# Kernel optimization log

Measured on AMD Instinct MI355X. Metric: run time of the kernel, lower is better.

The kernel has to match this reference:

```python
import jax, jax.numpy as jnp
import numpy as np

N_NODES = 100000
N_EDGES = 3200000
IN_CH = 512
HID = 16
OUT_CH = 2


def setup_inputs() -> dict:
    key = jax.random.key(0)
    k1, k2, k3, k4 = jax.random.split(key, 4)
    x = jax.random.normal(k1, (N_NODES, IN_CH), dtype=jnp.float32)
    edge_index = jax.random.randint(k2, (2, N_EDGES), 0, N_NODES, dtype=jnp.int32)
    # GCNConv weight (glorot-style scale) and zero bias; Linear xavier weight, zero bias
    W1 = jax.random.normal(k3, (IN_CH, HID), dtype=jnp.float32) * np.float32(np.sqrt(2.0 / (IN_CH + HID)))
    b1 = jnp.zeros((HID,), dtype=jnp.float32)
    W2 = jax.random.normal(k4, (HID, OUT_CH), dtype=jnp.float32) * np.float32(np.sqrt(2.0 / (HID + OUT_CH)))
    b2 = jnp.zeros((OUT_CH,), dtype=jnp.float32)
    return {"x": x, "edge_index": edge_index, "W1": W1, "b1": b1, "W2": W2, "b2": b2}


def reference(x, edge_index, W1, b1, W2, b2):
    # GCNConv with default add_self_loops=True, normalize=True:
    #   out = D^{-1/2} (A + I) D^{-1/2} X W1 + b1, then Linear(16, out).
    n = x.shape[0]
    loops = jnp.arange(n, dtype=edge_index.dtype)
    row = jnp.concatenate([edge_index[0], loops])  # source nodes j
    col = jnp.concatenate([edge_index[1], loops])  # target nodes i
    deg = jax.ops.segment_sum(jnp.ones_like(col, dtype=x.dtype), col, num_segments=n)
    dinv = jnp.where(deg > 0, jax.lax.rsqrt(deg), jnp.zeros_like(deg))
    norm = dinv[row] * dinv[col]  # [E+N]
    xw = x @ W1  # [N, 16] project first (PyG GCNConv order)
    agg = jax.ops.segment_sum(xw[row] * norm[:, None], col, num_segments=n)  # scatter-add to targets
    h = agg + b1
    return h @ W2 + b2  # [N, out_channels]
```

## Files before the change

kernel.cpp:

```cpp
#include <hip/hip_runtime.h>


constexpr int N_NODES = 100000;
constexpr int N_EDGES = 3200000;
constexpr int IN_CH   = 512;
constexpr int HID     = 16;
constexpr int OUT_CH  = 2;

constexpr int NBUCK      = (N_NODES + 255) / 256;
constexpr int BIN_BLOCKS = 320;
constexpr int EPB        = N_EDGES / BIN_BLOCKS;
constexpr int XW_BLOCKS  = N_NODES / 32;

typedef __attribute__((ext_vector_type(4))) float floatx4;


__global__ __launch_bounds__(1024) void k_count_wc(const int* __restrict__ tgt,
                                                   int* __restrict__ hist,
                                                   const float* __restrict__ W1,
                                                   const float* __restrict__ b1,
                                                   const float* __restrict__ W2,
                                                   const float* __restrict__ b2,
                                                   float* __restrict__ Wc,
                                                   float* __restrict__ bconst) {
    if (blockIdx.x == BIN_BLOCKS) {
        for (int i = threadIdx.x; i < IN_CH * OUT_CH; i += 1024) {
            int c = i >> 1, o = i & 1;
            float s = 0.f;
#pragma unroll
            for (int h = 0; h < HID; ++h) s += W1[c * HID + h] * W2[h * OUT_CH + o];
            Wc[i] = s;
        }
        if (threadIdx.x < OUT_CH) {
            float bo = b2[threadIdx.x];
#pragma unroll
            for (int h = 0; h < HID; ++h) bo += b1[h] * W2[h * OUT_CH + threadIdx.x];
            bconst[threadIdx.x] = bo;
        }
        return;
    }
    __shared__ int h[NBUCK];
    for (int i = threadIdx.x; i < NBUCK; i += 1024) h[i] = 0;
    __syncthreads();
    int e0 = blockIdx.x * EPB;
    for (int e = e0 + threadIdx.x; e < e0 + EPB; e += 1024)
        atomicAdd(&h[tgt[e] >> 8], 1);
    __syncthreads();
    for (int i = threadIdx.x; i < NBUCK; i += 1024)
        hist[blockIdx.x * NBUCK + i] = h[i];
}

__global__ __launch_bounds__(64) void k_colscan(int* __restrict__ hist,
                                                int* __restrict__ coltot) {
    int b = blockIdx.x;
    int lane = threadIdx.x;
    int v[5];
    int s = 0;
#pragma unroll
    for (int j = 0; j < 5; ++j) {
        v[j] = hist[(lane * 5 + j) * NBUCK + b];
        s += v[j];
    }
    int inc = s;
#pragma unroll
    for (int off = 1; off < 64; off <<= 1) {
        int n = __shfl_up(inc, off);
        if (lane >= off) inc += n;
    }
    int excl = inc - s;
#pragma unroll
    for (int j = 0; j < 5; ++j) {
        hist[(lane * 5 + j) * NBUCK + b] = excl;
        excl += v[j];
    }
    if (lane == 63) coltot[b] = inc;
}

__global__ __launch_bounds__(512) void k_basescan(const int* __restrict__ coltot,
                                                  int* __restrict__ bbase) {
    __shared__ int tmp[512];
    int tid = threadIdx.x;
    int v = (tid < NBUCK) ? coltot[tid] : 0;
    tmp[tid] = v;
    __syncthreads();
#pragma unroll
    for (int off = 1; off < 512; off <<= 1) {
        int tv = (tid >= off) ? tmp[tid - off] : 0;
        __syncthreads();
        tmp[tid] += tv;
        __syncthreads();
    }
    if (tid < NBUCK) bbase[tid] = tmp[tid] - v;
    if (tid == NBUCK - 1) bbase[NBUCK] = tmp[tid];
}

__global__ __launch_bounds__(1024) void k_bin_xw(const int* __restrict__ ei,
                                                 int* __restrict__ hist,
                                                 const int* __restrict__ bbase,
                                                 int* __restrict__ binned,
                                                 const float* __restrict__ x,
                                                 const float* __restrict__ Wc,
                                                 float2* __restrict__ t2) {
    if (blockIdx.x < BIN_BLOCKS) {
        __shared__ int lcur[NBUCK];
        int blk = blockIdx.x;
        for (int i = threadIdx.x; i < NBUCK; i += 1024)
            lcur[i] = bbase[i] + hist[blk * NBUCK + i];
        __syncthreads();
        int e0 = blk * EPB;
        for (int e = e0 + threadIdx.x; e < e0 + EPB; e += 1024) {
            int tg = ei[N_EDGES + e];
            int b = tg >> 8;
            int pos = atomicAdd(&lcur[b], 1);
            binned[pos] = ((tg & 255) << 20) | ei[e];
        }
        return;
    }
    int nb = blockIdx.x - BIN_BLOCKS;
    int wv = threadIdx.x >> 6;
    int lane = threadIdx.x & 63;
    int node = nb * 32 + wv * 2;
    const floatx4* xr0 = reinterpret_cast<const floatx4*>(
        x + (size_t)node * IN_CH + lane * 8);
    const floatx4* xr1 = reinterpret_cast<const floatx4*>(
        x + (size_t)(node + 1) * IN_CH + lane * 8);
    const floatx4* wr = reinterpret_cast<const floatx4*>(Wc + lane * 16);
    floatx4 a0 = xr0[0], a1 = xr0[1];
    floatx4 c0 = xr1[0], c1 = xr1[1];
    floatx4 w0 = wr[0], w1 = wr[1], w2 = wr[2], w3 = wr[3];
    float s0 = a0[0]*w0[0] + a0[1]*w0[2] + a0[2]*w1[0] + a0[3]*w1[2]
             + a1[0]*w2[0] + a1[1]*w2[2] + a1[2]*w3[0] + a1[3]*w3[2];
    float s1 = a0[0]*w0[1] + a0[1]*w0[3] + a0[2]*w1[1] + a0[3]*w1[3]
             + a1[0]*w2[1] + a1[1]*w2[3] + a1[2]*w3[1] + a1[3]*w3[3];
    float u0 = c0[0]*w0[0] + c0[1]*w0[2] + c0[2]*w1[0] + c0[3]*w1[2]
             + c1[0]*w2[0] + c1[1]*w2[2] + c1[2]*w3[0] + c1[3]*w3[2];
    float u1 = c0[0]*w0[1] + c0[1]*w0[3] + c0[2]*w1[1] + c0[3]*w1[3]
             + c1[0]*w2[1] + c1[1]*w2[3] + c1[2]*w3[1] + c1[3]*w3[3];
#pragma unroll
    for (int off = 32; off; off >>= 1) {
        s0 += __shfl_xor(s0, off);
        s1 += __shfl_xor(s1, off);
        u0 += __shfl_xor(u0, off);
        u1 += __shfl_xor(u1, off);
    }
    if (lane == 0) t2[node] = make_float2(s0, s1);
    else if (lane == 1) t2[node + 1] = make_float2(u0, u1);
}

__global__ __launch_bounds__(1024) void k_dinv(const int* __restrict__ bbase,
                                               const int* __restrict__ binned,
                                               float* __restrict__ dinv,
                                               float2* __restrict__ t2) {
    __shared__ int cnt[256];
    if (threadIdx.x < 256) cnt[threadIdx.x] = 0;
    __syncthreads();
    int b = blockIdx.x;
    int s = bbase[b], e = bbase[b + 1];
    for (int i = s + threadIdx.x; i < e; i += 1024)
        atomicAdd(&cnt[binned[i] >> 20], 1);
    __syncthreads();
    if (threadIdx.x < 256) {
        int node = (b << 8) + threadIdx.x;
        if (node < N_NODES) {
            float di = rsqrtf((float)(cnt[threadIdx.x] + 1));
            dinv[node] = di;
            float2 v = t2[node];
            t2[node] = make_float2(v.x * di, v.y * di);
        }
    }
}

__global__ __launch_bounds__(1024) void k_acc(const int* __restrict__ bbase,
                                              const int* __restrict__ binned,
                                              const float2* __restrict__ t2,
                                              const float* __restrict__ dinv,
                                              const float* __restrict__ bconst,
                                              float2* __restrict__ out) {
    __shared__ float acc0[256];
    __shared__ float acc1[256];
    if (threadIdx.x < 256) {
        acc0[threadIdx.x] = 0.f;
        acc1[threadIdx.x] = 0.f;
    }
    __syncthreads();
    int b = blockIdx.x;
    int s = bbase[b], e = bbase[b + 1];
    for (int i = s + threadIdx.x; i < e; i += 1024) {
        int v = binned[i];
        float2 ts = t2[v & 0xFFFFF];
        atomicAdd(&acc0[v >> 20], ts.x);
        atomicAdd(&acc1[v >> 20], ts.y);
    }
    __syncthreads();
    if (threadIdx.x < 256) {
        int node = (b << 8) + threadIdx.x;
        if (node < N_NODES) {
            float2 self = t2[node];
            float di = dinv[node];
            out[node] = make_float2(di * (acc0[threadIdx.x] + self.x) + bconst[0],
                                    di * (acc1[threadIdx.x] + self.y) + bconst[1]);
        }
    }
}

extern "C" void kernel_launch(void* const* d_in, const int* in_sizes, int n_in,
                              void* d_out, int out_size, void* d_ws, size_t ws_size,
                              hipStream_t stream) {
    const float* x  = (const float*)d_in[0];
    const int*   ei = (const int*)d_in[1];
    const float* W1 = (const float*)d_in[2];
    const float* b1 = (const float*)d_in[3];
    const float* W2 = (const float*)d_in[4];
    const float* b2 = (const float*)d_in[5];

    char* ws = (char*)d_ws;
    int*    hist   = (int*)   (ws + 0);
    int*    coltot = (int*)   (ws + 500480);
    int*    bbase  = (int*)   (ws + 502048);
    float*  Wc     = (float*) (ws + 503616);
    float*  bconst = (float*) (ws + 507712);
    float*  dinv   = (float*) (ws + 507728);
    float2* t2     = (float2*)(ws + 907728);
    int*    binned = (int*)   (ws + 1707728);

    k_count_wc<<<BIN_BLOCKS + 1, 1024, 0, stream>>>(ei + N_EDGES, hist,
                                                    W1, b1, W2, b2, Wc, bconst);
    k_colscan <<<NBUCK, 64, 0, stream>>>(hist, coltot);
    k_basescan<<<1, 512, 0, stream>>>(coltot, bbase);
    k_bin_xw  <<<BIN_BLOCKS + XW_BLOCKS, 1024, 0, stream>>>(ei, hist, bbase,
                                                            binned, x, Wc, t2);
    k_dinv    <<<NBUCK, 1024, 0, stream>>>(bbase, binned, dinv, t2);
    k_acc     <<<NBUCK, 1024, 0, stream>>>(bbase, binned, t2, dinv, bconst,
                                           (float2*)d_out);
}
```

Baseline: 384.7 us.

## Use finer 64-node buckets, fewer binning blocks, and four rows per wave in projection

Bucket width drops from 256 to 64 target nodes, which gives 1563 buckets. The binning stage now uses 128 blocks instead of 320, and both scans are rescaled to fit (two values per lane in the column scan, a 1024-thread base scan with two elements per thread). The degree and accumulation kernels launch 256-thread blocks over the smaller buckets, giving more blocks with less shared-memory atomic contention each. The projection kernel has each wave handle four nodes with clamped row indices. Trade-offs: a larger histogram, fewer binning blocks for parallelism, and a serial 11-step scan.

```diff
diff --git a/kernel.cpp b/kernel.cpp
--- a/kernel.cpp
+++ b/kernel.cpp
@@ -7,10 +7,12 @@
 constexpr int HID     = 16;
 constexpr int OUT_CH  = 2;
 
-constexpr int NBUCK      = (N_NODES + 255) / 256;
-constexpr int BIN_BLOCKS = 320;
+constexpr int BSHIFT = 6;
+constexpr int BSIZE  = 1 << BSHIFT;
+constexpr int NBUCK  = (N_NODES + BSIZE - 1) / BSIZE;
+constexpr int BIN_BLOCKS = 128;
 constexpr int EPB        = N_EDGES / BIN_BLOCKS;
-constexpr int XW_BLOCKS  = N_NODES / 32;
+constexpr int XW_BLOCKS  = (N_NODES + 63) / 64;
 
 typedef __attribute__((ext_vector_type(4))) float floatx4;
 
@@ -44,7 +46,7 @@
     __syncthreads();
     int e0 = blockIdx.x * EPB;
     for (int e = e0 + threadIdx.x; e < e0 + EPB; e += 1024)
-        atomicAdd(&h[tgt[e] >> 8], 1);
+        atomicAdd(&h[tgt[e] >> BSHIFT], 1);
     __syncthreads();
     for (int i = threadIdx.x; i < NBUCK; i += 1024)
         hist[blockIdx.x * NBUCK + i] = h[i];
@@ -54,11 +56,11 @@
                                                 int* __restrict__ coltot) {
     int b = blockIdx.x;
     int lane = threadIdx.x;
-    int v[5];
+    int v[2];
     int s = 0;
 #pragma unroll
-    for (int j = 0; j < 5; ++j) {
-        v[j] = hist[(lane * 5 + j) * NBUCK + b];
+    for (int j = 0; j < 2; ++j) {
+        v[j] = hist[(lane * 2 + j) * NBUCK + b];
         s += v[j];
     }
     int inc = s;
@@ -69,29 +71,33 @@
     }
     int excl = inc - s;
 #pragma unroll
-    for (int j = 0; j < 5; ++j) {
-        hist[(lane * 5 + j) * NBUCK + b] = excl;
+    for (int j = 0; j < 2; ++j) {
+        hist[(lane * 2 + j) * NBUCK + b] = excl;
         excl += v[j];
     }
     if (lane == 63) coltot[b] = inc;
 }
 
-__global__ __launch_bounds__(512) void k_basescan(const int* __restrict__ coltot,
-                                                  int* __restrict__ bbase) {
-    __shared__ int tmp[512];
+__global__ __launch_bounds__(1024) void k_basescan(const int* __restrict__ coltot,
+                                                   int* __restrict__ bbase) {
+    __shared__ int psum[1024];
     int tid = threadIdx.x;
-    int v = (tid < NBUCK) ? coltot[tid] : 0;
-    tmp[tid] = v;
-    __syncthreads();
-#pragma unroll
-    for (int off = 1; off < 512; off <<= 1) {
-        int tv = (tid >= off) ? tmp[tid - off] : 0;
+    int i0 = 2 * tid, i1 = 2 * tid + 1;
+    int v0 = (i0 < NBUCK) ? coltot[i0] : 0;
+    int v1 = (i1 < NBUCK) ? coltot[i1] : 0;
+    psum[tid] = v0 + v1;
+    __syncthreads();
+#pragma unroll
+    for (int off = 1; off < 1024; off <<= 1) {
+        int tv = (tid >= off) ? psum[tid - off] : 0;
         __syncthreads();
-        tmp[tid] += tv;
+        psum[tid] += tv;
         __syncthreads();
     }
-    if (tid < NBUCK) bbase[tid] = tmp[tid] - v;
-    if (tid == NBUCK - 1) bbase[NBUCK] = tmp[tid];
+    int excl = psum[tid] - (v0 + v1);
+    if (i0 < NBUCK) bbase[i0] = excl;
+    if (i1 < NBUCK) bbase[i1] = excl + v0;
+    if (tid == 1023) bbase[NBUCK] = psum[1023];
 }
 
 __global__ __launch_bounds__(1024) void k_bin_xw(const int* __restrict__ ei,
@@ -110,57 +116,75 @@
         int e0 = blk * EPB;
         for (int e = e0 + threadIdx.x; e < e0 + EPB; e += 1024) {
             int tg = ei[N_EDGES + e];
-            int b = tg >> 8;
+            int b = tg >> BSHIFT;
             int pos = atomicAdd(&lcur[b], 1);
-            binned[pos] = ((tg & 255) << 20) | ei[e];
+            binned[pos] = ((tg & (BSIZE - 1)) << 20) | ei[e];
         }
         return;
     }
     int nb = blockIdx.x - BIN_BLOCKS;
     int wv = threadIdx.x >> 6;
     int lane = threadIdx.x & 63;
-    int node = nb * 32 + wv * 2;
-    const floatx4* xr0 = reinterpret_cast<const floatx4*>(
-        x + (size_t)node * IN_CH + lane * 8);
-    const floatx4* xr1 = reinterpret_cast<const floatx4*>(
-        x + (size_t)(node + 1) * IN_CH + lane * 8);
+    int node = nb * 64 + wv * 4;
+    int r0 = min(node,     N_NODES - 1);
+    int r1 = min(node + 1, N_NODES - 1);
+    int r2 = min(node + 2, N_NODES - 1);
+    int r3 = min(node + 3, N_NODES - 1);
+    const floatx4* x0 = reinterpret_cast<const floatx4*>(x + (size_t)r0 * IN_CH + lane * 8);
+    const floatx4* x1 = reinterpret_cast<const floatx4*>(x + (size_t)r1 * IN_CH + lane * 8);
+    const floatx4* x2 = reinterpret_cast<const floatx4*>(x + (size_t)r2 * IN_CH + lane * 8);
+    const floatx4* x3 = reinterpret_cast<const floatx4*>(x + (size_t)r3 * IN_CH + lane * 8);
     const floatx4* wr = reinterpret_cast<const floatx4*>(Wc + lane * 16);
-    floatx4 a0 = xr0[0], a1 = xr0[1];
-    floatx4 c0 = xr1[0], c1 = xr1[1];
+    floatx4 a0 = x0[0], a1 = x0[1];
+    floatx4 b0 = x1[0], b1 = x1[1];
+    floatx4 c0 = x2[0], c1 = x2[1];
+    floatx4 d0 = x3[0], d1 = x3[1];
     floatx4 w0 = wr[0], w1 = wr[1], w2 = wr[2], w3 = wr[3];
-    float s0 = a0[0]*w0[0] + a0[1]*w0[2] + a0[2]*w1[0] + a0[3]*w1[2]
-             + a1[0]*w2[0] + a1[1]*w2[2] + a1[2]*w3[0] + a1[3]*w3[2];
-    float s1 = a0[0]*w0[1] + a0[1]*w0[3] + a0[2]*w1[1] + a0[3]*w1[3]
-             + a1[0]*w2[1] + a1[1]*w2[3] + a1[2]*w3[1] + a1[3]*w3[3];
-    float u0 = c0[0]*w0[0] + c0[1]*w0[2] + c0[2]*w1[0] + c0[3]*w1[2]
-             + c1[0]*w2[0] + c1[1]*w2[2] + c1[2]*w3[0] + c1[3]*w3[2];
-    float u1 = c0[0]*w0[1] + c0[1]*w0[3] + c0[2]*w1[1] + c0[3]*w1[3]
-             + c1[0]*w2[1] + c1[1]*w2[3] + c1[2]*w3[1] + c1[3]*w3[3];
+    float s0x = a0[0]*w0[0] + a0[1]*w0[2] + a0[2]*w1[0] + a0[3]*w1[2]
+              + a1[0]*w2[0] + a1[1]*w2[2] + a1[2]*w3[0] + a1[3]*w3[2];
+    float s0y = a0[0]*w0[1] + a0[1]*w0[3] + a0[2]*w1[1] + a0[3]*w1[3]
+              + a1[0]*w2[1] + a1[1]*w2[3] + a1[2]*w3[1] + a1[3]*w3[3];
+    float s1x = b0[0]*w0[0] + b0[1]*w0[2] + b0[2]*w1[0] + b0[3]*w1[2]
+              + b1[0]*w2[0] + b1[1]*w2[2] + b1[2]*w3[0] + b1[3]*w3[2];
+    float s1y = b0[0]*w0[1] + b0[1]*w0[3] + b0[2]*w1[1] + b0[3]*w1[3]
+              + b1[0]*w2[1] + b1[1]*w2[3] + b1[2]*w3[1] + b1[3]*w3[3];
+    float s2x = c0[0]*w0[0] + c0[1]*w0[2] + c0[2]*w1[0] + c0[3]*w1[2]
+              + c1[0]*w2[0] + c1[1]*w2[2] + c1[2]*w3[0] + c1[3]*w3[2];
+    float s2y = c0[0]*w0[1] + c0[1]*w0[3] + c0[2]*w1[1] + c0[3]*w1[3]
+              + c1[0]*w2[1] + c1[1]*w2[3] + c1[2]*w3[1] + c1[3]*w3[3];
+    float s3x = d0[0]*w0[0] + d0[1]*w0[2] + d0[2]*w1[0] + d0[3]*w1[2]
+              + d1[0]*w2[0] + d1[1]*w2[2] + d1[2]*w3[0] + d1[3]*w3[2];
+    float s3y = d0[0]*w0[1] + d0[1]*w0[3] + d0[2]*w1[1] + d0[3]*w1[3]
+              + d1[0]*w2[1] + d1[1]*w2[3] + d1[2]*w3[1] + d1[3]*w3[3];
 #pragma unroll
     for (int off = 32; off; off >>= 1) {
-        s0 += __shfl_xor(s0, off);
-        s1 += __shfl_xor(s1, off);
-        u0 += __shfl_xor(u0, off);
-        u1 += __shfl_xor(u1, off);
-    }
-    if (lane == 0) t2[node] = make_float2(s0, s1);
-    else if (lane == 1) t2[node + 1] = make_float2(u0, u1);
-}
-
-__global__ __launch_bounds__(1024) void k_dinv(const int* __restrict__ bbase,
-                                               const int* __restrict__ binned,
-                                               float* __restrict__ dinv,
-                                               float2* __restrict__ t2) {
-    __shared__ int cnt[256];
-    if (threadIdx.x < 256) cnt[threadIdx.x] = 0;
+        s0x += __shfl_xor(s0x, off); s0y += __shfl_xor(s0y, off);
+        s1x += __shfl_xor(s1x, off); s1y += __shfl_xor(s1y, off);
+        s2x += __shfl_xor(s2x, off); s2y += __shfl_xor(s2y, off);
+        s3x += __shfl_xor(s3x, off); s3y += __shfl_xor(s3y, off);
+    }
+    if (node + lane < N_NODES) {
+        if      (lane == 0) t2[node]     = make_float2(s0x, s0y);
+        else if (lane == 1) t2[node + 1] = make_float2(s1x, s1y);
+        else if (lane == 2) t2[node + 2] = make_float2(s2x, s2y);
+        else if (lane == 3) t2[node + 3] = make_float2(s3x, s3y);
+    }
+}
+
+__global__ __launch_bounds__(256) void k_dinv(const int* __restrict__ bbase,
+                                              const int* __restrict__ binned,
+                                              float* __restrict__ dinv,
+                                              float2* __restrict__ t2) {
+    __shared__ int cnt[BSIZE];
+    if (threadIdx.x < BSIZE) cnt[threadIdx.x] = 0;
     __syncthreads();
     int b = blockIdx.x;
     int s = bbase[b], e = bbase[b + 1];
-    for (int i = s + threadIdx.x; i < e; i += 1024)
+    for (int i = s + threadIdx.x; i < e; i += 256)
         atomicAdd(&cnt[binned[i] >> 20], 1);
     __syncthreads();
-    if (threadIdx.x < 256) {
-        int node = (b << 8) + threadIdx.x;
+    if (threadIdx.x < BSIZE) {
+        int node = (b << BSHIFT) + threadIdx.x;
         if (node < N_NODES) {
             float di = rsqrtf((float)(cnt[threadIdx.x] + 1));
             dinv[node] = di;
@@ -170,30 +194,30 @@
     }
 }
 
-__global__ __launch_bounds__(1024) void k_acc(const int* __restrict__ bbase,
-                                              const int* __restrict__ binned,
-                                              const float2* __restrict__ t2,
-                                              const float* __restrict__ dinv,
-                                              const float* __restrict__ bconst,
-                                              float2* __restrict__ out) {
-    __shared__ float acc0[256];
-    __shared__ float acc1[256];
-    if (threadIdx.x < 256) {
+__global__ __launch_bounds__(256) void k_acc(const int* __restrict__ bbase,
+                                             const int* __restrict__ binned,
+                                             const float2* __restrict__ t2,
+                                             const float* __restrict__ dinv,
+                                             const float* __restrict__ bconst,
+                                             float2* __restrict__ out) {
+    __shared__ float acc0[BSIZE];
+    __shared__ float acc1[BSIZE];
+    if (threadIdx.x < BSIZE) {
         acc0[threadIdx.x] = 0.f;
         acc1[threadIdx.x] = 0.f;
     }
     __syncthreads();
     int b = blockIdx.x;
     int s = bbase[b], e = bbase[b + 1];
-    for (int i = s + threadIdx.x; i < e; i += 1024) {
+    for (int i = s + threadIdx.x; i < e; i += 256) {
         int v = binned[i];
         float2 ts = t2[v & 0xFFFFF];
         atomicAdd(&acc0[v >> 20], ts.x);
         atomicAdd(&acc1[v >> 20], ts.y);
     }
     __syncthreads();
-    if (threadIdx.x < 256) {
-        int node = (b << 8) + threadIdx.x;
+    if (threadIdx.x < BSIZE) {
+        int node = (b << BSHIFT) + threadIdx.x;
         if (node < N_NODES) {
             float2 self = t2[node];
             float di = dinv[node];
@@ -215,21 +239,21 @@
 
     char* ws = (char*)d_ws;
     int*    hist   = (int*)   (ws + 0);
-    int*    coltot = (int*)   (ws + 500480);
-    int*    bbase  = (int*)   (ws + 502048);
-    float*  Wc     = (float*) (ws + 503616);
-    float*  bconst = (float*) (ws + 507712);
-    float*  dinv   = (float*) (ws + 507728);
-    float2* t2     = (float2*)(ws + 907728);
-    int*    binned = (int*)   (ws + 1707728);
+    int*    coltot = (int*)   (ws + 800256);
+    int*    bbase  = (int*)   (ws + 806512);
+    float*  Wc     = (float*) (ws + 812768);
+    float*  bconst = (float*) (ws + 816864);
+    float*  dinv   = (float*) (ws + 816880);
+    float2* t2     = (float2*)(ws + 1216880);
+    int*    binned = (int*)   (ws + 2016896);
 
     k_count_wc<<<BIN_BLOCKS + 1, 1024, 0, stream>>>(ei + N_EDGES, hist,
                                                     W1, b1, W2, b2, Wc, bconst);
     k_colscan <<<NBUCK, 64, 0, stream>>>(hist, coltot);
-    k_basescan<<<1, 512, 0, stream>>>(coltot, bbase);
+    k_basescan<<<1, 1024, 0, stream>>>(coltot, bbase);
     k_bin_xw  <<<BIN_BLOCKS + XW_BLOCKS, 1024, 0, stream>>>(ei, hist, bbase,
                                                             binned, x, Wc, t2);
-    k_dinv    <<<NBUCK, 1024, 0, stream>>>(bbase, binned, dinv, t2);
-    k_acc     <<<NBUCK, 1024, 0, stream>>>(bbase, binned, t2, dinv, bconst,
-                                           (float2*)d_out);
-}
+    k_dinv    <<<NBUCK, 256, 0, stream>>>(bbase, binned, dinv, t2);
+    k_acc     <<<NBUCK, 256, 0, stream>>>(bbase, binned, t2, dinv, bconst,
+                                          (float2*)d_out);
+}
```

Measured after the change: 405.6 us. +5.4%, slower.

## Stage binned edges in LDS for coalesced writes; process four nodes per wave

Applied to the files above, without the earlier changes.

The binning blocks now first scatter edges into a shared-memory staging buffer ordered by bucket, using a local prefix scan of each block's per-bucket counts. Each wave then copies contiguous bucket runs to global memory, replacing random scattered 4-byte global stores with coalesced ones. The x·Wc projection part now handles four nodes per wave instead of two, halving the block count and adding bounds clamps. Costs: roughly 40KB of extra LDS per binning block, an extra in-block scan, and more registers in the projection path.

```diff
diff --git a/kernel.cpp b/kernel.cpp
--- a/kernel.cpp
+++ b/kernel.cpp
@@ -10,7 +10,7 @@
 constexpr int NBUCK      = (N_NODES + 255) / 256;
 constexpr int BIN_BLOCKS = 320;
 constexpr int EPB        = N_EDGES / BIN_BLOCKS;
-constexpr int XW_BLOCKS  = N_NODES / 32;
+constexpr int XW_BLOCKS  = (N_NODES + 63) / 64;
 
 typedef __attribute__((ext_vector_type(4))) float floatx4;
 
@@ -95,56 +95,107 @@
 }
 
 __global__ __launch_bounds__(1024) void k_bin_xw(const int* __restrict__ ei,
-                                                 int* __restrict__ hist,
+                                                 const int* __restrict__ hist,
+                                                 const int* __restrict__ coltot,
                                                  const int* __restrict__ bbase,
                                                  int* __restrict__ binned,
                                                  const float* __restrict__ x,
                                                  const float* __restrict__ Wc,
                                                  float2* __restrict__ t2) {
     if (blockIdx.x < BIN_BLOCKS) {
+        __shared__ int goff[NBUCK];
+        __shared__ int rlen[NBUCK];
+        __shared__ int lofs[512];
         __shared__ int lcur[NBUCK];
+        __shared__ int stage[EPB];
         int blk = blockIdx.x;
-        for (int i = threadIdx.x; i < NBUCK; i += 1024)
-            lcur[i] = bbase[i] + hist[blk * NBUCK + i];
+        int tid = threadIdx.x;
+        for (int b = tid; b < NBUCK; b += 1024) {
+            int g  = hist[blk * NBUCK + b];
+            int nx = (blk == BIN_BLOCKS - 1) ? coltot[b]
+                                             : hist[(blk + 1) * NBUCK + b];
+            goff[b] = g;
+            rlen[b] = nx - g;
+        }
+        __syncthreads();
+        if (tid < 512) lofs[tid] = (tid < NBUCK) ? rlen[tid] : 0;
+        __syncthreads();
+#pragma unroll
+        for (int off = 1; off < 512; off <<= 1) {
+            int tv = 0;
+            if (tid < 512 && tid >= off) tv = lofs[tid - off];
+            __syncthreads();
+            if (tid < 512) lofs[tid] += tv;
+            __syncthreads();
+        }
+        for (int b = tid; b < NBUCK; b += 1024)
+            lcur[b] = lofs[b] - rlen[b];
         __syncthreads();
         int e0 = blk * EPB;
-        for (int e = e0 + threadIdx.x; e < e0 + EPB; e += 1024) {
+        for (int e = e0 + tid; e < e0 + EPB; e += 1024) {
             int tg = ei[N_EDGES + e];
             int b = tg >> 8;
-            int pos = atomicAdd(&lcur[b], 1);
-            binned[pos] = ((tg & 255) << 20) | ei[e];
+            int lpos = atomicAdd(&lcur[b], 1);
+            stage[lpos] = ((tg & 255) << 20) | ei[e];
+        }
+        __syncthreads();
+        int wv = tid >> 6, lane = tid & 63;
+        for (int b = wv; b < NBUCK; b += 16) {
+            int len = rlen[b];
+            int gbase = bbase[b] + goff[b];
+            int lbase = lofs[b] - len;
+            for (int i = lane; i < len; i += 64)
+                binned[gbase + i] = stage[lbase + i];
         }
         return;
     }
     int nb = blockIdx.x - BIN_BLOCKS;
     int wv = threadIdx.x >> 6;
     int lane = threadIdx.x & 63;
-    int node = nb * 32 + wv * 2;
-    const floatx4* xr0 = reinterpret_cast<const floatx4*>(
-        x + (size_t)node * IN_CH + lane * 8);
-    const floatx4* xr1 = reinterpret_cast<const floatx4*>(
-        x + (size_t)(node + 1) * IN_CH + lane * 8);
+    int node = nb * 64 + wv * 4;
+    int r0 = min(node,     N_NODES - 1);
+    int r1 = min(node + 1, N_NODES - 1);
+    int r2 = min(node + 2, N_NODES - 1);
+    int r3 = min(node + 3, N_NODES - 1);
+    const floatx4* x0 = reinterpret_cast<const floatx4*>(x + (size_t)r0 * IN_CH + lane * 8);
+    const floatx4* x1 = reinterpret_cast<const floatx4*>(x + (size_t)r1 * IN_CH + lane * 8);
+    const floatx4* x2 = reinterpret_cast<const floatx4*>(x + (size_t)r2 * IN_CH + lane * 8);
+    const floatx4* x3 = reinterpret_cast<const floatx4*>(x + (size_t)r3 * IN_CH + lane * 8);
     const floatx4* wr = reinterpret_cast<const floatx4*>(Wc + lane * 16);
-    floatx4 a0 = xr0[0], a1 = xr0[1];
-    floatx4 c0 = xr1[0], c1 = xr1[1];
+    floatx4 a0 = x0[0], a1 = x0[1];
+    floatx4 b0 = x1[0], b1 = x1[1];
+    floatx4 c0 = x2[0], c1 = x2[1];
+    floatx4 d0 = x3[0], d1 = x3[1];
     floatx4 w0 = wr[0], w1 = wr[1], w2 = wr[2], w3 = wr[3];
-    float s0 = a0[0]*w0[0] + a0[1]*w0[2] + a0[2]*w1[0] + a0[3]*w1[2]
-             + a1[0]*w2[0] + a1[1]*w2[2] + a1[2]*w3[0] + a1[3]*w3[2];
-    float s1 = a0[0]*w0[1] + a0[1]*w0[3] + a0[2]*w1[1] + a0[3]*w1[3]
-             + a1[0]*w2[1] + a1[1]*w2[3] + a1[2]*w3[1] + a1[3]*w3[3];
-    float u0 = c0[0]*w0[0] + c0[1]*w0[2] + c0[2]*w1[0] + c0[3]*w1[2]
-             + c1[0]*w2[0] + c1[1]*w2[2] + c1[2]*w3[0] + c1[3]*w3[2];
-    float u1 = c0[0]*w0[1] + c0[1]*w0[3] + c0[2]*w1[1] + c0[3]*w1[3]
-             + c1[0]*w2[1] + c1[1]*w2[3] + c1[2]*w3[1] + c1[3]*w3[3];
+    float s0x = a0[0]*w0[0] + a0[1]*w0[2] + a0[2]*w1[0] + a0[3]*w1[2]
+              + a1[0]*w2[0] + a1[1]*w2[2] + a1[2]*w3[0] + a1[3]*w3[2];
+    float s0y = a0[0]*w0[1] + a0[1]*w0[3] + a0[2]*w1[1] + a0[3]*w1[3]
+              + a1[0]*w2[1] + a1[1]*w2[3] + a1[2]*w3[1] + a1[3]*w3[3];
+    float s1x = b0[0]*w0[0] + b0[1]*w0[2] + b0[2]*w1[0] + b0[3]*w1[2]
+              + b1[0]*w2[0] + b1[1]*w2[2] + b1[2]*w3[0] + b1[3]*w3[2];
+    float s1y = b0[0]*w0[1] + b0[1]*w0[3] + b0[2]*w1[1] + b0[3]*w1[3]
+              + b1[0]*w2[1] + b1[1]*w2[3] + b1[2]*w3[1] + b1[3]*w3[3];
+    float s2x = c0[0]*w0[0] + c0[1]*w0[2] + c0[2]*w1[0] + c0[3]*w1[2]
+              + c1[0]*w2[0] + c1[1]*w2[2] + c1[2]*w3[0] + c1[3]*w3[2];
+    float s2y = c0[0]*w0[1] + c0[1]*w0[3] + c0[2]*w1[1] + c0[3]*w1[3]
+              + c1[0]*w2[1] + c1[1]*w2[3] + c1[2]*w3[1] + c1[3]*w3[3];
+    float s3x = d0[0]*w0[0] + d0[1]*w0[2] + d0[2]*w1[0] + d0[3]*w1[2]
+              + d1[0]*w2[0] + d1[1]*w2[2] + d1[2]*w3[0] + d1[3]*w3[2];
+    float s3y = d0[0]*w0[1] + d0[1]*w0[3] + d0[2]*w1[1] + d0[3]*w1[3]
+              + d1[0]*w2[1] + d1[1]*w2[3] + d1[2]*w3[1] + d1[3]*w3[3];
 #pragma unroll
     for (int off = 32; off; off >>= 1) {
-        s0 += __shfl_xor(s0, off);
-        s1 += __shfl_xor(s1, off);
-        u0 += __shfl_xor(u0, off);
-        u1 += __shfl_xor(u1, off);
-    }
-    if (lane == 0) t2[node] = make_float2(s0, s1);
-    else if (lane == 1) t2[node + 1] = make_float2(u0, u1);
+        s0x += __shfl_xor(s0x, off); s0y += __shfl_xor(s0y, off);
+        s1x += __shfl_xor(s1x, off); s1y += __shfl_xor(s1y, off);
+        s2x += __shfl_xor(s2x, off); s2y += __shfl_xor(s2y, off);
+        s3x += __shfl_xor(s3x, off); s3y += __shfl_xor(s3y, off);
+    }
+    if (node + lane < N_NODES) {
+        if      (lane == 0) t2[node]     = make_float2(s0x, s0y);
+        else if (lane == 1) t2[node + 1] = make_float2(s1x, s1y);
+        else if (lane == 2) t2[node + 2] = make_float2(s2x, s2y);
+        else if (lane == 3) t2[node + 3] = make_float2(s3x, s3y);
+    }
 }
 
 __global__ __launch_bounds__(1024) void k_dinv(const int* __restrict__ bbase,
@@ -227,8 +278,9 @@
                                                     W1, b1, W2, b2, Wc, bconst);
     k_colscan <<<NBUCK, 64, 0, stream>>>(hist, coltot);
     k_basescan<<<1, 512, 0, stream>>>(coltot, bbase);
-    k_bin_xw  <<<BIN_BLOCKS + XW_BLOCKS, 1024, 0, stream>>>(ei, hist, bbase,
-                                                            binned, x, Wc, t2);
+    k_bin_xw  <<<BIN_BLOCKS + XW_BLOCKS, 1024, 0, stream>>>(ei, hist, coltot,
+                                                            bbase, binned,
+                                                            x, Wc, t2);
     k_dinv    <<<NBUCK, 1024, 0, stream>>>(bbase, binned, dinv, t2);
     k_acc     <<<NBUCK, 1024, 0, stream>>>(bbase, binned, t2, dinv, bconst,
                                            (float2*)d_out);
```

Measured after the change: 371.4 us. 1.04x faster.
